# Optimization experiments

Hardware: AMD Instinct MI355X
Metric: run time of the kernel (lower is better)

The kernel has to match this reference:

```python
import jax, jax.numpy as jnp
import numpy as np

N = 100000; E = 1600000; IN = 64; H = 128; G = 64

def setup_inputs() -> dict:
    key = jax.random.key(0)
    ks = jax.random.split(key, 8)
    h = jax.random.normal(ks[0], (N, IN), jnp.float32)
    src = jax.random.randint(ks[1], (E,), 0, N, jnp.int32)
    dst = jax.random.randint(ks[2], (E,), 0, N, jnp.int32)
    graph_ids = jnp.sort(jax.random.randint(ks[3], (N,), 0, G, jnp.int32))
    W1 = jax.random.normal(ks[4], (IN, H), jnp.float32) / jnp.sqrt(IN)
    b1 = jnp.zeros((H,), jnp.float32)
    W2 = jax.random.normal(ks[5], (H, H), jnp.float32) / jnp.sqrt(H)
    b2 = jnp.zeros((H,), jnp.float32)
    Wr = jax.random.normal(ks[6], (H, 1), jnp.float32) / jnp.sqrt(H)
    br = jnp.zeros((1,), jnp.float32)
    return {"h": h, "src": src, "dst": dst, "graph_ids": graph_ids, "num_graphs": G,
            "W1": W1, "b1": b1, "W2": W2, "b2": b2, "Wr": Wr, "br": br}

def _gcn(x, src, dst, inv_sqrt_out, inv_sqrt_in, W, b):
    # DGL GraphConv, norm='both', aggregate-first (in_feats <= out_feats):
    # out = D_in^{-1/2} * A * (D_out^{-1/2} * x) @ W + b
    x = x * inv_sqrt_out[:, None]
    agg = jax.ops.segment_sum(x[src], dst, num_segments=x.shape[0])  # [N, d]
    return agg @ W * inv_sqrt_in[:, None] + b

def reference(h, src, dst, graph_ids, num_graphs, W1, b1, W2, b2, Wr, br):
    n = h.shape[0]
    ones_e = jnp.ones(src.shape[0], h.dtype)
    deg_out = jnp.maximum(jax.ops.segment_sum(ones_e, src, num_segments=n), 1.0)
    deg_in = jnp.maximum(jax.ops.segment_sum(ones_e, dst, num_segments=n), 1.0)
    iso = jax.lax.rsqrt(deg_out)
    isi = jax.lax.rsqrt(deg_in)
    h1 = jax.nn.relu(_gcn(h, src, dst, iso, isi, W1, b1))   # conv1 has activation=relu
    h2 = _gcn(h1, src, dst, iso, isi, W2, b2)               # conv2 has no activation
    hf = jax.nn.relu(h2)                                    # outer F.relu in forward
    # mean_nodes: per-graph mean readout
    sums = jax.ops.segment_sum(hf, graph_ids, num_segments=num_graphs)  # [G, H]
    cnt = jnp.maximum(jax.ops.segment_sum(jnp.ones(n, hf.dtype), graph_ids, num_segments=num_graphs), 1.0)
    hg = sums / cnt[:, None]
    return hg @ Wr + br  # [G, 1]
```

## Files before the change

### kernel.cpp

```cpp
#include <hip/hip_runtime.h>

#define N_IN 64
#define N_H  128
#define N_G  64
#define HP   4
#define HC   64
#define YSTRIDE 132

#define SWZB(r) (((r) & 7) << 3)

typedef unsigned int   uint32;
typedef unsigned short ushort16;
typedef unsigned char  uchar8;
typedef float floatx2 __attribute__((ext_vector_type(2)));
typedef short bf16x8 __attribute__((ext_vector_type(8)));
typedef float f32x4  __attribute__((ext_vector_type(4)));

#define FP8_SCALE    32.0f
#define FP8_INVSCALE 0.03125f

#if defined(__has_builtin)
#if __has_builtin(__builtin_amdgcn_cvt_pk_f32_fp8) && __has_builtin(__builtin_amdgcn_cvt_pk_fp8_f32)
#define HW_FP8 1
#endif
#endif

__device__ __forceinline__ float bf2f(ushort16 u) {
    union { uint32 i; float f; } x; x.i = ((uint32)u) << 16; return x.f;
}
__device__ __forceinline__ ushort16 f2bf(float f) {
    union { float f; uint32 i; } x; x.f = f;
    uint32 r = x.i + 0x7FFFu + ((x.i >> 16) & 1u);
    return (ushort16)(r >> 16);
}

#ifndef HW_FP8
__device__ __forceinline__ uint32 f2e4m3(float x) {
    union { float f; uint32 i; } v; v.f = x;
    uint32 s = (v.i >> 24) & 0x80u;
    uint32 a = v.i & 0x7FFFFFFFu;
    if (a < 0x3C000000u) return s;
    uint32 r = a + 0x0007FFFFu + ((a >> 20) & 1u);
    int e = (int)(r >> 23) - 120;
    if (e <= 0) return s;
    if (e > 15) return s | 0x7Eu;
    return s | ((uint32)e << 3) | ((r >> 20) & 7u);
}
__device__ __forceinline__ floatx2 e4m3word(uint32 u, bool hi) {
    floatx2 o;
    uint32 w = hi ? (u >> 16) : u;
    #pragma unroll
    for (int k = 0; k < 2; ++k) {
        uint32 b = (w >> (8 * k)) & 0xFFu;
        uint32 m = b & 0x7Fu;
        union { uint32 i; float f; } x;
        x.i = ((b & 0x80u) << 24) | ((m << 20) + 0x3C000000u);
        o[k] = m ? x.f : 0.f;
    }
    return o;
}
#endif

__device__ __forceinline__ floatx2 fp8lo(uint32 u) {
#ifdef HW_FP8
    return __builtin_amdgcn_cvt_pk_f32_fp8((int)u, false);
#else
    return e4m3word(u, false);
#endif
}
__device__ __forceinline__ floatx2 fp8hi(uint32 u) {
#ifdef HW_FP8
    return __builtin_amdgcn_cvt_pk_f32_fp8((int)u, true);
#else
    return e4m3word(u, true);
#endif
}

__device__ __forceinline__ uint32 pack4fp8(float o0, float o1, float o2, float o3) {
#ifdef HW_FP8
    int r = __builtin_amdgcn_cvt_pk_fp8_f32(o0, o1, 0, false);
    r     = __builtin_amdgcn_cvt_pk_fp8_f32(o2, o3, r, true);
    return (uint32)r;
#else
    return f2e4m3(o0) | (f2e4m3(o1) << 8) | (f2e4m3(o2) << 16) | (f2e4m3(o3) << 24);
#endif
}


__global__ __launch_bounds__(1024) void hist_kernel(const int* __restrict__ src,
        const int* __restrict__ dst, ushort16* __restrict__ part_cnt,
        int N, int E, int npp, int ec) {
    extern __shared__ int cnt[];
    int p = blockIdx.x & (HP - 1);
    int c = blockIdx.x >> 2;
    int nlo = p * npp;
    int nhi = min(nlo + npp, N);
    int nn = nhi - nlo;
    if (nn <= 0) return;
    int tid = threadIdx.x;
    for (int i = tid; i < nn; i += 1024) cnt[i] = 0;
    __syncthreads();
    int elo = c * ec, ehi = min(elo + ec, E);
    for (int e = elo + tid; e < ehi; e += 1024) {
        int s = src[e];
        unsigned so = (unsigned)(s - nlo);
        if (so < (unsigned)nn) atomicAdd(&cnt[so], 1);
        int d = dst[e];
        unsigned dof = (unsigned)(d - nlo);
        if (dof < (unsigned)nn) atomicAdd(&cnt[dof], 1 << 16);
    }
    __syncthreads();
    for (int i = tid; i < nn; i += 1024) {
        int v = cnt[i];
        part_cnt[(size_t)c * N + nlo + i] =
            (ushort16)((v & 0xFF) | ((v >> 8) & 0xFF00));
    }
}

__global__ void reduce_norm_kernel(const ushort16* __restrict__ part_cnt,
        uchar8* __restrict__ pre, const int* __restrict__ gid,
        float* __restrict__ iso, float* __restrict__ isi, int* __restrict__ deg_in,
        int* __restrict__ gstart, int* __restrict__ gend, int N) {
    int n = blockIdx.x * blockDim.x + threadIdx.x;
    if (n >= N) return;
    int so = 0, si = 0;
    #pragma unroll
    for (int c = 0; c < HC; ++c) {
        int v = part_cnt[(size_t)c * N + n];
        so += v & 0xFF;
        pre[(size_t)c * N + n] = (uchar8)si;
        si += v >> 8;
    }
    iso[n] = rsqrtf((float)max(so, 1));
    isi[n] = rsqrtf((float)max(si, 1));
    deg_in[n] = si;
    int g = gid[n];
    if (n == 0 || gid[n - 1] != g) gstart[g] = n;
    if (n == N - 1 || gid[n + 1] != g) gend[g] = n + 1;
}

__global__ __launch_bounds__(1024) void scan_partial(const int* __restrict__ deg_in,
                                                     int* __restrict__ bsum, int N) {
    int i = blockIdx.x * 1024 + threadIdx.x;
    int v = (i < N) ? deg_in[i] : 0;
    int lane = threadIdx.x & 63, wv = threadIdx.x >> 6;
    int s = v;
    #pragma unroll
    for (int off = 1; off < 64; off <<= 1) s += __shfl_xor(s, off);
    __shared__ int ws[16];
    if (lane == 0) ws[wv] = s;
    __syncthreads();
    if (threadIdx.x == 0) {
        int t = 0;
        #pragma unroll
        for (int k = 0; k < 16; ++k) t += ws[k];
        bsum[blockIdx.x] = t;
    }
}

__global__ void scan_bsum(int* __restrict__ bsum, int nb) {
    int tid = threadIdx.x;
    int lane = tid & 63, wv = tid >> 6;
    int v = (tid < nb) ? bsum[tid] : 0;
    int s = v;
    #pragma unroll
    for (int off = 1; off < 64; off <<= 1) {
        int t = __shfl_up(s, off);
        if (lane >= off) s += t;
    }
    __shared__ int w0tot;
    if (wv == 0 && lane == 63) w0tot = s;
    __syncthreads();
    if (wv == 1) s += w0tot;
    if (tid < nb) bsum[tid] = s - v;
}

__global__ __launch_bounds__(1024) void scan_write(const int* __restrict__ deg_in,
                                                   const int* __restrict__ bsum,
                                                   int* __restrict__ row_ptr, int N) {
    int i = blockIdx.x * 1024 + threadIdx.x;
    int v = (i < N) ? deg_in[i] : 0;
    int lane = threadIdx.x & 63, wv = threadIdx.x >> 6;
    int s = v;
    #pragma unroll
    for (int off = 1; off < 64; off <<= 1) {
        int t = __shfl_up(s, off);
        if (lane >= off) s += t;
    }
    __shared__ int ws[16];
    if (lane == 63) ws[wv] = s;
    __syncthreads();
    if (wv == 0 && lane < 16) {
        int x = ws[lane];
        int s2 = x;
        #pragma unroll
        for (int off = 1; off < 16; off <<= 1) {
            int t = __shfl_up(s2, off);
            if (lane >= off) s2 += t;
        }
        ws[lane] = s2;
    }
    __syncthreads();
    int base = bsum[blockIdx.x] + (wv > 0 ? ws[wv - 1] : 0);
    if (i < N) row_ptr[i] = base + s - v;
    if (i == N - 1) row_ptr[N] = base + s;
}

__global__ __launch_bounds__(1024) void fill_kernel(const int* __restrict__ src,
        const int* __restrict__ dst, const int* __restrict__ row_ptr,
        const uchar8* __restrict__ pre, int* __restrict__ col,
        int N, int E, int npp, int ec) {
    extern __shared__ int cur[];
    int p = blockIdx.x & (HP - 1);
    int c = blockIdx.x >> 2;
    int nlo = p * npp;
    int nhi = min(nlo + npp, N);
    int nn = nhi - nlo;
    if (nn <= 0) return;
    int tid = threadIdx.x;
    for (int i = tid; i < nn; i += 1024)
        cur[i] = row_ptr[nlo + i] + (int)pre[(size_t)c * N + nlo + i];
    __syncthreads();
    int elo = c * ec, ehi = min(elo + ec, E);
    for (int e = elo + tid; e < ehi; e += 1024) {
        int d = dst[e];
        unsigned off = (unsigned)(d - nlo);
        if (off < (unsigned)nn) {
            int slot = atomicAdd(&cur[off], 1);
            col[slot] = src[e];
        }
    }
}

__global__ __launch_bounds__(256) void scale_h_kernel(const float* __restrict__ h,
        const float* __restrict__ iso, uchar8* __restrict__ hs8, int N) {
    int t = blockIdx.x * 256 + threadIdx.x;
    int base = t * 8;
    if (base >= N * N_IN) return;
    int n = base >> 6;
    float s = iso[n] * FP8_SCALE;
    float4 a = *(const float4*)&h[base];
    float4 b = *(const float4*)&h[base + 4];
    uint2 pk;
    pk.x = pack4fp8(a.x * s, a.y * s, a.z * s, a.w * s);
    pk.y = pack4fp8(b.x * s, b.y * s, b.z * s, b.w * s);
    *(uint2*)&hs8[base] = pk;
}

__global__ __launch_bounds__(1024) void wprep_kernel(const float* __restrict__ W1,
        const float* __restrict__ W2, ushort16* __restrict__ W1T,
        ushort16* __restrict__ W2T, int* __restrict__ zbase, int zero_words) {
    int t = blockIdx.x * 1024 + threadIdx.x;
    if (t < zero_words) zbase[t] = 0;
    if (t < 128 * 128) {
        int j = t >> 7, k = t & 127;
        W2T[j * 128 + k] = f2bf(W2[k * 128 + j]);
    } else if (t < 128 * 128 + 128 * 64) {
        int q = t - 128 * 128;
        int j = q >> 6, k = q & 63;
        W1T[j * 64 + k] = f2bf(W1[k * 128 + j]);
    }
}

__global__ __launch_bounds__(256) void gather1_kernel(const uchar8* __restrict__ hs8,
        const int* __restrict__ row_ptr, const int* __restrict__ col,
        uint32* __restrict__ agg1w, int N) {
    int wave = __builtin_amdgcn_readfirstlane(threadIdx.x >> 6);
    int lane = threadIdx.x & 63;
    int qd = lane >> 4, l16 = lane & 15;
    int n = blockIdx.x * 4 + wave;
    if (n >= N) return;
    int p0 = row_ptr[n], p1 = row_ptr[n + 1];
    uint32 lofs = (uint32)l16 * 4;
    float a0 = 0.f, a1 = 0.f, a2 = 0.f, a3 = 0.f;
    for (int pb = p0; pb < p1; pb += 64) {
        int cnt = min(64, p1 - pb);
        uint32 cvoff = ((uint32)col[min(pb + lane, p1 - 1)]) << 6;
        int i0 = 0;
        for (; i0 + 16 <= cnt; i0 += 16) {
            uint32 off[4], u[4];
            #pragma unroll
            for (int i = 0; i < 4; ++i)
                off[i] = __shfl(cvoff, i0 + 4 * i + qd);
            #pragma unroll
            for (int i = 0; i < 4; ++i)
                u[i] = *(const uint32*)((const char*)hs8 + (off[i] + lofs));
            #pragma unroll
            for (int i = 0; i < 4; ++i) {
                floatx2 dlo = fp8lo(u[i]), dhi = fp8hi(u[i]);
                a0 += dlo.x; a1 += dlo.y; a2 += dhi.x; a3 += dhi.y;
            }
        }
        if (i0 < cnt) {
            uint32 off[4], u[4];
            float w[4];
            #pragma unroll
            for (int i = 0; i < 4; ++i) {
                int q = i0 + 4 * i + qd;
                off[i] = __shfl(cvoff, min(q, cnt - 1));
                w[i] = (q < cnt) ? 1.f : 0.f;
            }
            #pragma unroll
            for (int i = 0; i < 4; ++i)
                u[i] = *(const uint32*)((const char*)hs8 + (off[i] + lofs));
            #pragma unroll
            for (int i = 0; i < 4; ++i) {
                floatx2 dlo = fp8lo(u[i]), dhi = fp8hi(u[i]);
                a0 = fmaf(dlo.x, w[i], a0);
                a1 = fmaf(dlo.y, w[i], a1);
                a2 = fmaf(dhi.x, w[i], a2);
                a3 = fmaf(dhi.y, w[i], a3);
            }
        }
    }
    a0 += __shfl_xor(a0, 16); a0 += __shfl_xor(a0, 32);
    a1 += __shfl_xor(a1, 16); a1 += __shfl_xor(a1, 32);
    a2 += __shfl_xor(a2, 16); a2 += __shfl_xor(a2, 32);
    a3 += __shfl_xor(a3, 16); a3 += __shfl_xor(a3, 32);
    if (lane < 16) {
        a0 *= FP8_INVSCALE; a1 *= FP8_INVSCALE; a2 *= FP8_INVSCALE; a3 *= FP8_INVSCALE;
        uint32 w0 = (uint32)f2bf(a0) | ((uint32)f2bf(a1) << 16);
        uint32 w1 = (uint32)f2bf(a2) | ((uint32)f2bf(a3) << 16);
        *(uint2*)&agg1w[(size_t)n * 32 + l16 * 2] = uint2{w0, w1};
    }
}

__global__ __launch_bounds__(256) void gather2_kernel(const uchar8* __restrict__ h18,
        const int* __restrict__ row_ptr, const int* __restrict__ col,
        uint32* __restrict__ agg2w, int N) {
    int wave = __builtin_amdgcn_readfirstlane(threadIdx.x >> 6);
    int lane = threadIdx.x & 63;
    int half = lane >> 5, l32 = lane & 31;
    int n = blockIdx.x * 4 + wave;
    if (n >= N) return;
    int p0 = row_ptr[n], p1 = row_ptr[n + 1];
    uint32 lofs = (uint32)l32 * 4;
    float a0 = 0.f, a1 = 0.f, a2 = 0.f, a3 = 0.f;
    for (int pb = p0; pb < p1; pb += 64) {
        int cnt = min(64, p1 - pb);
        uint32 cvoff = ((uint32)col[min(pb + lane, p1 - 1)]) << 7;
        int i0 = 0;
        for (; i0 + 16 <= cnt; i0 += 16) {
            uint32 off[8], u[8];
            #pragma unroll
            for (int i = 0; i < 8; ++i)
                off[i] = __shfl(cvoff, i0 + 2 * i + half);
            #pragma unroll
            for (int i = 0; i < 8; ++i)
                u[i] = *(const uint32*)((const char*)h18 + (off[i] + lofs));
            #pragma unroll
            for (int i = 0; i < 8; ++i) {
                floatx2 dlo = fp8lo(u[i]), dhi = fp8hi(u[i]);
                a0 += dlo.x; a1 += dlo.y; a2 += dhi.x; a3 += dhi.y;
            }
        }
        if (i0 < cnt) {
            uint32 off[8], u[8];
            float w[8];
            #pragma unroll
            for (int i = 0; i < 8; ++i) {
                int q = i0 + 2 * i + half;
                off[i] = __shfl(cvoff, min(q, cnt - 1));
                w[i] = (q < cnt) ? 1.f : 0.f;
            }
            #pragma unroll
            for (int i = 0; i < 8; ++i)
                u[i] = *(const uint32*)((const char*)h18 + (off[i] + lofs));
            #pragma unroll
            for (int i = 0; i < 8; ++i) {
                floatx2 dlo = fp8lo(u[i]), dhi = fp8hi(u[i]);
                a0 = fmaf(dlo.x, w[i], a0);
                a1 = fmaf(dlo.y, w[i], a1);
                a2 = fmaf(dhi.x, w[i], a2);
                a3 = fmaf(dhi.y, w[i], a3);
            }
        }
    }
    a0 += __shfl_xor(a0, 32);
    a1 += __shfl_xor(a1, 32);
    a2 += __shfl_xor(a2, 32);
    a3 += __shfl_xor(a3, 32);
    if (half == 0) {
        a0 *= FP8_INVSCALE; a1 *= FP8_INVSCALE; a2 *= FP8_INVSCALE; a3 *= FP8_INVSCALE;
        uint32 w0 = (uint32)f2bf(a0) | ((uint32)f2bf(a1) << 16);
        uint32 w1 = (uint32)f2bf(a2) | ((uint32)f2bf(a3) << 16);
        *(uint2*)&agg2w[(size_t)n * 64 + l32 * 2] = uint2{w0, w1};
    }
}

__global__ __launch_bounds__(512) void mm1_kernel(const ushort16* __restrict__ agg1bf,
        const ushort16* __restrict__ W1T, const float* __restrict__ b1,
        const float* __restrict__ isi, const float* __restrict__ iso,
        uchar8* __restrict__ h18, int N) {
    __shared__ union {
        struct { ushort16 A[128 * 64]; ushort16 W[128 * 64]; } st;
        float Y[128 * YSTRIDE];
    } u;
    __shared__ float ISI[128], ISO[128];
    int t = threadIdx.x;
    int n0 = blockIdx.x * 128;
    {
        int r = t >> 2;
        int k0 = (t & 3) * 16;
        bool valid = (n0 + r) < N;
        const uint4* ga = (const uint4*)(agg1bf + (size_t)(n0 + r) * 64 + k0);
        const uint4* gw = (const uint4*)(W1T + (size_t)r * 64 + k0);
        #pragma unroll
        for (int q = 0; q < 2; ++q) {
            uint4 va = valid ? ga[q] : uint4{0, 0, 0, 0};
            uint4 vw = gw[q];
            int kg = k0 + q * 8;
            *(uint4*)&u.st.A[r * 64 + (kg ^ SWZB(r))] = va;
            *(uint4*)&u.st.W[r * 64 + (kg ^ SWZB(r))] = vw;
        }
        if (t < 128) {
            ISI[t] = (n0 + t < N) ? isi[n0 + t] : 0.f;
            ISO[t] = (n0 + t < N) ? iso[n0 + t] * FP8_SCALE : 0.f;
        }
    }
    __syncthreads();
    int w = __builtin_amdgcn_readfirstlane(t >> 6);
    int l = t & 63, l15 = l & 15, lhi = l >> 4;
    int jcol = w * 16 + l15;
    float b1j = b1[jcol];
    f32x4 acc[8] = {};
    #pragma unroll
    for (int kk = 0; kk < 2; ++kk) {
        int kb = kk * 32 + lhi * 8;
        bf16x8 bf = *(bf16x8*)&u.st.W[jcol * 64 + (kb ^ SWZB(jcol))];
        #pragma unroll
        for (int tm = 0; tm < 8; ++tm) {
            int row = tm * 16 + l15;
            bf16x8 af = *(bf16x8*)&u.st.A[row * 64 + (kb ^ SWZB(row))];
            acc[tm] = __builtin_amdgcn_mfma_f32_16x16x32_bf16(af, bf, acc[tm], 0, 0, 0);
        }
    }
    __syncthreads();
    #pragma unroll
    for (int tm = 0; tm < 8; ++tm) {
        #pragma unroll
        for (int i = 0; i < 4; ++i) {
            int m = tm * 16 + lhi * 4 + i;
            u.Y[m * YSTRIDE + jcol] =
                fmaxf(fmaf(acc[tm][i], ISI[m], b1j), 0.f) * ISO[m];
        }
    }
    __syncthreads();
    {
        int r = t >> 2;
        int c0 = (t & 3) * 32;
        if (n0 + r < N) {
            uint32 b[8];
            #pragma unroll
            for (int q = 0; q < 8; ++q) {
                float4 y4 = *(float4*)&u.Y[r * YSTRIDE + c0 + q * 4];
                b[q] = pack4fp8(y4.x, y4.y, y4.z, y4.w);
            }
            uchar8* dstp = h18 + (size_t)(n0 + r) * 128 + c0;
            *(uint4*)dstp        = uint4{b[0], b[1], b[2], b[3]};
            *(uint4*)(dstp + 16) = uint4{b[4], b[5], b[6], b[7]};
        }
    }
}

__global__ __launch_bounds__(512) void mm2_kernel(const uint32* __restrict__ agg2bf,
        const ushort16* __restrict__ W2T, const float* __restrict__ b2,
        const float* __restrict__ isi, const int* __restrict__ gid,
        float* __restrict__ sums, int N) {
    __shared__ union {
        struct { ushort16 A[128 * 128]; ushort16 W[128 * 128]; } st;
        float Y[128 * YSTRIDE];
    } u;
    __shared__ float ISI[128];
    int t = threadIdx.x;
    int n0 = blockIdx.x * 128;
    {
        int r = t >> 2;
        int k0 = (t & 3) * 32;
        bool valid = (n0 + r) < N;
        const uint4* ga = (const uint4*)((const ushort16*)agg2bf + (size_t)(n0 + r) * 128 + k0);
        const uint4* gw = (const uint4*)(W2T + (size_t)r * 128 + k0);
        #pragma unroll
        for (int q = 0; q < 4; ++q) {
            uint4 va = valid ? ga[q] : uint4{0, 0, 0, 0};
            uint4 vw = gw[q];
            int kg = k0 + q * 8;
            *(uint4*)&u.st.A[r * 128 + (kg ^ SWZB(r))] = va;
            *(uint4*)&u.st.W[r * 128 + (kg ^ SWZB(r))] = vw;
        }
        if (t < 128) ISI[t] = (n0 + t < N) ? isi[n0 + t] : 0.f;
    }
    __syncthreads();
    int w = __builtin_amdgcn_readfirstlane(t >> 6);
    int l = t & 63, l15 = l & 15, lhi = l >> 4;
    int jcol = w * 16 + l15;
    float b2j = b2[jcol];
    f32x4 acc[8] = {};
    #pragma unroll
    for (int kk = 0; kk < 4; ++kk) {
        int kb = kk * 32 + lhi * 8;
        bf16x8 bf = *(bf16x8*)&u.st.W[jcol * 128 + (kb ^ SWZB(jcol))];
        #pragma unroll
        for (int tm = 0; tm < 8; ++tm) {
            int row = tm * 16 + l15;
            bf16x8 af = *(bf16x8*)&u.st.A[row * 128 + (kb ^ SWZB(row))];
            acc[tm] = __builtin_amdgcn_mfma_f32_16x16x32_bf16(af, bf, acc[tm], 0, 0, 0);
        }
    }
    __syncthreads();
    #pragma unroll
    for (int tm = 0; tm < 8; ++tm) {
        #pragma unroll
        for (int i = 0; i < 4; ++i) {
            int m = tm * 16 + lhi * 4 + i;
            u.Y[m * YSTRIDE + jcol] = fmaxf(fmaf(acc[tm][i], ISI[m], b2j), 0.f);
        }
    }
    __syncthreads();
    int j = t & 127;
    int seg = t >> 7;
    float racc = 0.f;
    int cur = -1;
    for (int i = 0; i < 32; ++i) {
        int ln = seg * 32 + i;
        int n = n0 + ln;
        if (n >= N) break;
        float y = u.Y[ln * YSTRIDE + j];
        int g = gid[n];
        if (g != cur) {
            if (cur >= 0) atomicAdd(&sums[cur * N_H + j], racc);
            racc = 0.f;
            cur = g;
        }
        racc += y;
    }
    if (cur >= 0) atomicAdd(&sums[cur * N_H + j], racc);
}

__global__ void out_kernel(const float* __restrict__ sums, const int* __restrict__ gstart,
                           const int* __restrict__ gend, const float* __restrict__ Wr,
                           const float* __restrict__ br, float* __restrict__ out) {
    int g = blockIdx.x;
    int j = threadIdx.x;
    float c = fmaxf((float)(gend[g] - gstart[g]), 1.f);
    float v = sums[g * N_H + j] / c * Wr[j];
    for (int off = 32; off > 0; off >>= 1) v += __shfl_down(v, off);
    __shared__ float part[2];
    if ((threadIdx.x & 63) == 0) part[threadIdx.x >> 6] = v;
    __syncthreads();
    if (threadIdx.x == 0) out[g] = part[0] + part[1] + br[0];
}

static inline size_t align_up(size_t x, size_t a) { return (x + a - 1) & ~(a - 1); }

extern "C" void kernel_launch(void* const* d_in, const int* in_sizes, int n_in,
                              void* d_out, int out_size, void* d_ws, size_t ws_size,
                              hipStream_t stream) {
    const float* h  = (const float*)d_in[0];
    const int* src  = (const int*)d_in[1];
    const int* dst  = (const int*)d_in[2];
    const int* gid  = (const int*)d_in[3];
    const float* W1 = (const float*)d_in[5];
    const float* b1 = (const float*)d_in[6];
    const float* W2 = (const float*)d_in[7];
    const float* b2 = (const float*)d_in[8];
    const float* Wr = (const float*)d_in[9];
    const float* br = (const float*)d_in[10];
    float* out = (float*)d_out;

    int N = in_sizes[0] / N_IN;
    int E = in_sizes[1];
    int nb  = (N + 1023) / 1024;
    int npp = (N + HP - 1) / HP;
    int ec  = (E + HC - 1) / HC;
    size_t hist_lds = (size_t)npp * 4;

    char* ws = (char*)d_ws;
    size_t off = 0;
    auto alloc = [&](size_t bytes) -> char* {
        char* p = ws + off;
        off = align_up(off + bytes, 256);
        return p;
    };
    int*   gstart  = (int*)alloc((size_t)N_G * 4);
    int*   gend    = (int*)alloc((size_t)N_G * 4);
    float* sums    = (float*)alloc((size_t)N_G * N_H * 4);
    size_t zero_bytes = off;
    int zero_words = (int)(zero_bytes / 4);
    int*      deg_in  = (int*)alloc((size_t)N * 4);
    float*    iso     = (float*)alloc((size_t)N * 4);
    float*    isi     = (float*)alloc((size_t)N * 4);
    int*      row_ptr = (int*)alloc((size_t)(N + 1) * 4);
    int*      bsum    = (int*)alloc((size_t)128 * 4);
    int*      col     = (int*)alloc((size_t)E * 4);
    uchar8*   hs8     = (uchar8*)alloc((size_t)N * N_IN);
    uchar8*   h18     = (uchar8*)alloc((size_t)N * N_H);
    ushort16* W1T     = (ushort16*)alloc((size_t)128 * 64 * 2);
    ushort16* W2T     = (ushort16*)alloc((size_t)128 * 128 * 2);
    ushort16* agg1bf  = (ushort16*)alloc((size_t)N * N_IN * 2);
    uint32*   agg2bf  = (uint32*)alloc((size_t)N * 64 * 4);
    ushort16* part_cnt = (ushort16*)agg1bf;
    uchar8*   pre      = (uchar8*)agg2bf;

    wprep_kernel<<<24, 1024, 0, stream>>>(W1, W2, W1T, W2T, (int*)d_ws, zero_words);
    hist_kernel<<<HP * HC, 1024, hist_lds, stream>>>(src, dst, part_cnt, N, E, npp, ec);
    reduce_norm_kernel<<<(N + 255) / 256, 256, 0, stream>>>(part_cnt, pre, gid, iso, isi,
                                                            deg_in, gstart, gend, N);
    scan_partial<<<nb, 1024, 0, stream>>>(deg_in, bsum, N);
    scan_bsum<<<1, 128, 0, stream>>>(bsum, nb);
    scan_write<<<nb, 1024, 0, stream>>>(deg_in, bsum, row_ptr, N);
    fill_kernel<<<HP * HC, 1024, hist_lds, stream>>>(src, dst, row_ptr, pre, col, N, E, npp, ec);
    scale_h_kernel<<<(N * N_IN / 8 + 255) / 256, 256, 0, stream>>>(h, iso, hs8, N);

    gather1_kernel<<<(N + 3) / 4, 256, 0, stream>>>(hs8, row_ptr, col, (uint32*)agg1bf, N);
    mm1_kernel<<<(N + 127) / 128, 512, 0, stream>>>(agg1bf, W1T, b1, isi, iso, h18, N);
    gather2_kernel<<<(N + 3) / 4, 256, 0, stream>>>(h18, row_ptr, col, agg2bf, N);
    mm2_kernel<<<(N + 127) / 128, 512, 0, stream>>>(agg2bf, W2T, b2, isi, gid, sums, N);
    out_kernel<<<N_G, N_H, 0, stream>>>(sums, gstart, gend, Wr, br, out);
}
```

Baseline: 187.9 us.

## Fuse small setup kernels to cut launch count and merge scan stages

Weight transposition and workspace zeroing are folded into extra blocks of the histogram kernel. The block-sum step of the scan is merged into the degree-reduction kernel. The scan write is merged with the fp8 scaling of h, with each scan block summing its own prefix of block totals. The final readout is folded into mm2 through a last-block-done atomic counter. Together these replace five launches with fewer fused ones, at the cost of redundant prefix summation in each scan block and a grid-wide completion counter.

```diff
diff --git a/kernel.cpp b/kernel.cpp
--- a/kernel.cpp
+++ b/kernel.cpp
@@ -86,13 +86,29 @@
 #endif
 }
 
-
 __global__ __launch_bounds__(1024) void hist_kernel(const int* __restrict__ src,
         const int* __restrict__ dst, ushort16* __restrict__ part_cnt,
+        const float* __restrict__ W1, const float* __restrict__ W2,
+        ushort16* __restrict__ W1T, ushort16* __restrict__ W2T,
+        int* __restrict__ zbase, int zero_words,
         int N, int E, int npp, int ec) {
     extern __shared__ int cnt[];
-    int p = blockIdx.x & (HP - 1);
-    int c = blockIdx.x >> 2;
+    int b = blockIdx.x;
+    if (b >= HP * HC) {
+        int base = (b - HP * HC) * 1024 + threadIdx.x;
+        for (int t = base; t < zero_words; t += 8 * 1024) zbase[t] = 0;
+        for (int t = base; t < 128 * 128; t += 8 * 1024) {
+            int j = t >> 7, k = t & 127;
+            W2T[j * 128 + k] = f2bf(W2[k * 128 + j]);
+        }
+        for (int t = base; t < 128 * 64; t += 8 * 1024) {
+            int j = t >> 6, k = t & 63;
+            W1T[j * 64 + k] = f2bf(W1[k * 128 + j]);
+        }
+        return;
+    }
+    int p = b & (HP - 1);
+    int c = b >> 2;
     int nlo = p * npp;
     int nhi = min(nlo + npp, N);
     int nn = nhi - nlo;
@@ -117,93 +133,83 @@
     }
 }
 
-__global__ void reduce_norm_kernel(const ushort16* __restrict__ part_cnt,
+__global__ __launch_bounds__(256) void reduce_norm_kernel(const ushort16* __restrict__ part_cnt,
         uchar8* __restrict__ pre, const int* __restrict__ gid,
         float* __restrict__ iso, float* __restrict__ isi, int* __restrict__ deg_in,
-        int* __restrict__ gstart, int* __restrict__ gend, int N) {
-    int n = blockIdx.x * blockDim.x + threadIdx.x;
-    if (n >= N) return;
-    int so = 0, si = 0;
-    #pragma unroll
-    for (int c = 0; c < HC; ++c) {
-        int v = part_cnt[(size_t)c * N + n];
-        so += v & 0xFF;
-        pre[(size_t)c * N + n] = (uchar8)si;
-        si += v >> 8;
-    }
-    iso[n] = rsqrtf((float)max(so, 1));
-    isi[n] = rsqrtf((float)max(si, 1));
-    deg_in[n] = si;
-    int g = gid[n];
-    if (n == 0 || gid[n - 1] != g) gstart[g] = n;
-    if (n == N - 1 || gid[n + 1] != g) gend[g] = n + 1;
-}
-
-__global__ __launch_bounds__(1024) void scan_partial(const int* __restrict__ deg_in,
-                                                     int* __restrict__ bsum, int N) {
-    int i = blockIdx.x * 1024 + threadIdx.x;
-    int v = (i < N) ? deg_in[i] : 0;
+        int* __restrict__ gstart, int* __restrict__ gend, int* __restrict__ bsum, int N) {
+    int n = blockIdx.x * 256 + threadIdx.x;
+    int si = 0;
+    if (n < N) {
+        int so = 0;
+        #pragma unroll
+        for (int c = 0; c < HC; ++c) {
+            int v = part_cnt[(size_t)c * N + n];
+            so += v & 0xFF;
+            pre[(size_t)c * N + n] = (uchar8)si;
+            si += v >> 8;
+        }
+        iso[n] = rsqrtf((float)max(so, 1));
+        isi[n] = rsqrtf((float)max(si, 1));
+        deg_in[n] = si;
+        int g = gid[n];
+        if (n == 0 || gid[n - 1] != g) gstart[g] = n;
+        if (n == N - 1 || gid[n + 1] != g) gend[g] = n + 1;
+    }
     int lane = threadIdx.x & 63, wv = threadIdx.x >> 6;
-    int s = v;
+    int s = si;
     #pragma unroll
     for (int off = 1; off < 64; off <<= 1) s += __shfl_xor(s, off);
-    __shared__ int ws[16];
+    __shared__ int ws[4];
     if (lane == 0) ws[wv] = s;
     __syncthreads();
-    if (threadIdx.x == 0) {
-        int t = 0;
-        #pragma unroll
-        for (int k = 0; k < 16; ++k) t += ws[k];
-        bsum[blockIdx.x] = t;
-    }
-}
-
-__global__ void scan_bsum(int* __restrict__ bsum, int nb) {
+    if (threadIdx.x == 0) bsum[blockIdx.x] = ws[0] + ws[1] + ws[2] + ws[3];
+}
+
+__global__ __launch_bounds__(256) void scanw_scaleh_kernel(const int* __restrict__ deg_in,
+        const int* __restrict__ bsum, int* __restrict__ row_ptr,
+        const float* __restrict__ h, const float* __restrict__ iso,
+        uchar8* __restrict__ hs8, int nb2, int N) {
+    int b = blockIdx.x;
     int tid = threadIdx.x;
-    int lane = tid & 63, wv = tid >> 6;
-    int v = (tid < nb) ? bsum[tid] : 0;
-    int s = v;
-    #pragma unroll
-    for (int off = 1; off < 64; off <<= 1) {
-        int t = __shfl_up(s, off);
-        if (lane >= off) s += t;
-    }
-    __shared__ int w0tot;
-    if (wv == 0 && lane == 63) w0tot = s;
-    __syncthreads();
-    if (wv == 1) s += w0tot;
-    if (tid < nb) bsum[tid] = s - v;
-}
-
-__global__ __launch_bounds__(1024) void scan_write(const int* __restrict__ deg_in,
-                                                   const int* __restrict__ bsum,
-                                                   int* __restrict__ row_ptr, int N) {
-    int i = blockIdx.x * 1024 + threadIdx.x;
-    int v = (i < N) ? deg_in[i] : 0;
-    int lane = threadIdx.x & 63, wv = threadIdx.x >> 6;
-    int s = v;
-    #pragma unroll
-    for (int off = 1; off < 64; off <<= 1) {
-        int t = __shfl_up(s, off);
-        if (lane >= off) s += t;
-    }
-    __shared__ int ws[16];
-    if (lane == 63) ws[wv] = s;
-    __syncthreads();
-    if (wv == 0 && lane < 16) {
-        int x = ws[lane];
-        int s2 = x;
-        #pragma unroll
-        for (int off = 1; off < 16; off <<= 1) {
-            int t = __shfl_up(s2, off);
-            if (lane >= off) s2 += t;
-        }
-        ws[lane] = s2;
-    }
-    __syncthreads();
-    int base = bsum[blockIdx.x] + (wv > 0 ? ws[wv - 1] : 0);
-    if (i < N) row_ptr[i] = base + s - v;
-    if (i == N - 1) row_ptr[N] = base + s;
+    if (b < nb2) {
+        int lane = tid & 63, wv = tid >> 6;
+        int acc = 0;
+        for (int i = tid; i < b; i += 256) acc += bsum[i];
+        #pragma unroll
+        for (int off = 1; off < 64; off <<= 1) acc += __shfl_xor(acc, off);
+        __shared__ int wsum[4];
+        if (lane == 0) wsum[wv] = acc;
+        __syncthreads();
+        int base = wsum[0] + wsum[1] + wsum[2] + wsum[3];
+        int n = b * 256 + tid;
+        int v = (n < N) ? deg_in[n] : 0;
+        int s = v;
+        #pragma unroll
+        for (int off = 1; off < 64; off <<= 1) {
+            int t2 = __shfl_up(s, off);
+            if (lane >= off) s += t2;
+        }
+        __shared__ int winc[4];
+        if (lane == 63) winc[wv] = s;
+        __syncthreads();
+        int wpre = 0;
+        #pragma unroll
+        for (int k = 0; k < 4; ++k) wpre += (k < wv) ? winc[k] : 0;
+        if (n < N) row_ptr[n] = base + wpre + s - v;
+        if (n == N - 1) row_ptr[N] = base + wpre + s;
+    } else {
+        int t = (b - nb2) * 256 + tid;
+        int base = t * 8;
+        if (base >= N * N_IN) return;
+        int n = base >> 6;
+        float sc = iso[n] * FP8_SCALE;
+        float4 a = *(const float4*)&h[base];
+        float4 bb = *(const float4*)&h[base + 4];
+        uint2 pk;
+        pk.x = pack4fp8(a.x * sc, a.y * sc, a.z * sc, a.w * sc);
+        pk.y = pack4fp8(bb.x * sc, bb.y * sc, bb.z * sc, bb.w * sc);
+        *(uint2*)&hs8[base] = pk;
+    }
 }
 
 __global__ __launch_bounds__(1024) void fill_kernel(const int* __restrict__ src,
@@ -229,36 +235,6 @@
             int slot = atomicAdd(&cur[off], 1);
             col[slot] = src[e];
         }
-    }
-}
-
-__global__ __launch_bounds__(256) void scale_h_kernel(const float* __restrict__ h,
-        const float* __restrict__ iso, uchar8* __restrict__ hs8, int N) {
-    int t = blockIdx.x * 256 + threadIdx.x;
-    int base = t * 8;
-    if (base >= N * N_IN) return;
-    int n = base >> 6;
-    float s = iso[n] * FP8_SCALE;
-    float4 a = *(const float4*)&h[base];
-    float4 b = *(const float4*)&h[base + 4];
-    uint2 pk;
-    pk.x = pack4fp8(a.x * s, a.y * s, a.z * s, a.w * s);
-    pk.y = pack4fp8(b.x * s, b.y * s, b.z * s, b.w * s);
-    *(uint2*)&hs8[base] = pk;
-}
-
-__global__ __launch_bounds__(1024) void wprep_kernel(const float* __restrict__ W1,
-        const float* __restrict__ W2, ushort16* __restrict__ W1T,
-        ushort16* __restrict__ W2T, int* __restrict__ zbase, int zero_words) {
-    int t = blockIdx.x * 1024 + threadIdx.x;
-    if (t < zero_words) zbase[t] = 0;
-    if (t < 128 * 128) {
-        int j = t >> 7, k = t & 127;
-        W2T[j * 128 + k] = f2bf(W2[k * 128 + j]);
-    } else if (t < 128 * 128 + 128 * 64) {
-        int q = t - 128 * 128;
-        int j = q >> 6, k = q & 63;
-        W1T[j * 64 + k] = f2bf(W1[k * 128 + j]);
     }
 }
 
@@ -466,7 +442,10 @@
 __global__ __launch_bounds__(512) void mm2_kernel(const uint32* __restrict__ agg2bf,
         const ushort16* __restrict__ W2T, const float* __restrict__ b2,
         const float* __restrict__ isi, const int* __restrict__ gid,
-        float* __restrict__ sums, int N) {
+        float* __restrict__ sums, const int* __restrict__ gstart,
+        const int* __restrict__ gend, const float* __restrict__ Wr,
+        const float* __restrict__ br, float* __restrict__ out,
+        int* __restrict__ done, int N) {
     __shared__ union {
         struct { ushort16 A[128 * 128]; ushort16 W[128 * 128]; } st;
         float Y[128 * YSTRIDE];
@@ -535,20 +514,26 @@
         racc += y;
     }
     if (cur >= 0) atomicAdd(&sums[cur * N_H + j], racc);
-}
-
-__global__ void out_kernel(const float* __restrict__ sums, const int* __restrict__ gstart,
-                           const int* __restrict__ gend, const float* __restrict__ Wr,
-                           const float* __restrict__ br, float* __restrict__ out) {
-    int g = blockIdx.x;
-    int j = threadIdx.x;
-    float c = fmaxf((float)(gend[g] - gstart[g]), 1.f);
-    float v = sums[g * N_H + j] / c * Wr[j];
-    for (int off = 32; off > 0; off >>= 1) v += __shfl_down(v, off);
-    __shared__ float part[2];
-    if ((threadIdx.x & 63) == 0) part[threadIdx.x >> 6] = v;
-    __syncthreads();
-    if (threadIdx.x == 0) out[g] = part[0] + part[1] + br[0];
+    __threadfence();
+    __syncthreads();
+    __shared__ int isLast;
+    if (t == 0) isLast = (atomicAdd(done, 1) == (int)gridDim.x - 1) ? 1 : 0;
+    __syncthreads();
+    if (isLast) {
+        int lane = t & 63;
+        int wv8 = t >> 6;
+        for (int g = wv8; g < N_G; g += 8) {
+            float c = fmaxf((float)(gend[g] - gstart[g]), 1.f);
+            float s0 = __hip_atomic_load(&sums[g * N_H + lane],
+                                         __ATOMIC_RELAXED, __HIP_MEMORY_SCOPE_AGENT);
+            float s1 = __hip_atomic_load(&sums[g * N_H + lane + 64],
+                                         __ATOMIC_RELAXED, __HIP_MEMORY_SCOPE_AGENT);
+            float v = (s0 * Wr[lane] + s1 * Wr[lane + 64]) / c;
+            #pragma unroll
+            for (int off = 32; off > 0; off >>= 1) v += __shfl_down(v, off);
+            if (lane == 0) out[g] = v + br[0];
+        }
+    }
 }
 
 static inline size_t align_up(size_t x, size_t a) { return (x + a - 1) & ~(a - 1); }
@@ -570,7 +555,7 @@
 
     int N = in_sizes[0] / N_IN;
     int E = in_sizes[1];
-    int nb  = (N + 1023) / 1024;
+    int nb2 = (N + 255) / 256;
     int npp = (N + HP - 1) / HP;
     int ec  = (E + HC - 1) / HC;
     size_t hist_lds = (size_t)npp * 4;
@@ -585,13 +570,14 @@
     int*   gstart  = (int*)alloc((size_t)N_G * 4);
     int*   gend    = (int*)alloc((size_t)N_G * 4);
     float* sums    = (float*)alloc((size_t)N_G * N_H * 4);
+    int*   done    = (int*)alloc(4);
     size_t zero_bytes = off;
     int zero_words = (int)(zero_bytes / 4);
     int*      deg_in  = (int*)alloc((size_t)N * 4);
     float*    iso     = (float*)alloc((size_t)N * 4);
     float*    isi     = (float*)alloc((size_t)N * 4);
     int*      row_ptr = (int*)alloc((size_t)(N + 1) * 4);
-    int*      bsum    = (int*)alloc((size_t)128 * 4);
+    int*      bsum    = (int*)alloc((size_t)512 * 4);
     int*      col     = (int*)alloc((size_t)E * 4);
     uchar8*   hs8     = (uchar8*)alloc((size_t)N * N_IN);
     uchar8*   h18     = (uchar8*)alloc((size_t)N * N_H);
@@ -602,19 +588,18 @@
     ushort16* part_cnt = (ushort16*)agg1bf;
     uchar8*   pre      = (uchar8*)agg2bf;
 
-    wprep_kernel<<<24, 1024, 0, stream>>>(W1, W2, W1T, W2T, (int*)d_ws, zero_words);
-    hist_kernel<<<HP * HC, 1024, hist_lds, stream>>>(src, dst, part_cnt, N, E, npp, ec);
-    reduce_norm_kernel<<<(N + 255) / 256, 256, 0, stream>>>(part_cnt, pre, gid, iso, isi,
-                                                            deg_in, gstart, gend, N);
-    scan_partial<<<nb, 1024, 0, stream>>>(deg_in, bsum, N);
-    scan_bsum<<<1, 128, 0, stream>>>(bsum, nb);
-    scan_write<<<nb, 1024, 0, stream>>>(deg_in, bsum, row_ptr, N);
+    int sc_blocks = (N * N_IN / 8 + 255) / 256;
+
+    hist_kernel<<<HP * HC + 8, 1024, hist_lds, stream>>>(src, dst, part_cnt,
+            W1, W2, W1T, W2T, (int*)d_ws, zero_words, N, E, npp, ec);
+    reduce_norm_kernel<<<nb2, 256, 0, stream>>>(part_cnt, pre, gid, iso, isi,
+            deg_in, gstart, gend, bsum, N);
+    scanw_scaleh_kernel<<<nb2 + sc_blocks, 256, 0, stream>>>(deg_in, bsum, row_ptr,
+            h, iso, hs8, nb2, N);
     fill_kernel<<<HP * HC, 1024, hist_lds, stream>>>(src, dst, row_ptr, pre, col, N, E, npp, ec);
-    scale_h_kernel<<<(N * N_IN / 8 + 255) / 256, 256, 0, stream>>>(h, iso, hs8, N);
-
     gather1_kernel<<<(N + 3) / 4, 256, 0, stream>>>(hs8, row_ptr, col, (uint32*)agg1bf, N);
     mm1_kernel<<<(N + 127) / 128, 512, 0, stream>>>(agg1bf, W1T, b1, isi, iso, h18, N);
     gather2_kernel<<<(N + 3) / 4, 256, 0, stream>>>(h18, row_ptr, col, agg2bf, N);
-    mm2_kernel<<<(N + 127) / 128, 512, 0, stream>>>(agg2bf, W2T, b2, isi, gid, sums, N);
-    out_kernel<<<N_G, N_H, 0, stream>>>(sums, gstart, gend, Wr, br, out);
-}
+    mm2_kernel<<<(N + 127) / 128, 512, 0, stream>>>(agg2bf, W2T, b2, isi, gid, sums,
+            gstart, gend, Wr, br, out, done, N);
+}
```

New measurement: 267.3 us. +42.3%, slower.
